# Performance work log

Hardware: AMD Instinct MI355X
Metric: run time of the kernel (lower is better)

The kernel has to match this reference:

```python
import jax, jax.numpy as jnp
import numpy as np

LN_EPS = 1e-5


def setup_inputs() -> dict:
    key = jax.random.key(0)
    ks = jax.random.split(key, 5)
    L, G, D, E = 2, 50000, 128, 800000
    x = jax.random.normal(ks[0], (L, G, D), dtype=jnp.float32)
    rows = jax.random.randint(ks[1], (E,), 0, G, dtype=jnp.int32)
    cols = jax.random.randint(ks[2], (E,), 0, G, dtype=jnp.int32)
    vals = jax.random.uniform(ks[3], (E,), dtype=jnp.float32)
    W = jax.random.normal(ks[4], (D, D), dtype=jnp.float32) * 0.05
    b = jnp.zeros((D,), dtype=jnp.float32)
    gamma = jnp.ones((D,), dtype=jnp.float32)
    beta = jnp.zeros((D,), dtype=jnp.float32)
    return {"x": x, "rows": rows, "cols": cols, "vals": vals,
            "W": W, "b": b, "gamma": gamma, "beta": beta}


def reference(x, rows, cols, vals, W, b, gamma, beta):
    L, G, D = x.shape
    # sparse connection_matrix @ x, edge-list form (COO): out[r] += v * x_t[c]
    xt = x.transpose(1, 0, 2).reshape(G, L * D)          # [G, L*D]
    msg = xt[cols] * vals[:, None]                        # [E, L*D]
    agg = jax.ops.segment_sum(msg, rows, num_segments=G)  # [G, L*D]
    y = agg.reshape(G, L, D).transpose(1, 0, 2)           # [L, G, D]
    # linear + SiLU
    h = jnp.einsum('lgd,od->lgo', y, W) + b
    s = h * jax.nn.sigmoid(h)
    # LayerNorm over last dim
    mu = jnp.mean(s, axis=-1, keepdims=True)
    var = jnp.mean(jnp.square(s - mu), axis=-1, keepdims=True)
    out = (s - mu) * jax.lax.rsqrt(var + LN_EPS) * gamma + beta
    return out
```

## Files before the change

### kernel.cpp

```cpp
#include <hip/hip_runtime.h>
#include <hip/hip_bf16.h>
#include <math.h>

typedef short bf16x8 __attribute__((ext_vector_type(8)));
typedef float f32x4 __attribute__((ext_vector_type(4)));

#define SPW 2
#define CAP 64
#define CSTR 16

static __device__ __forceinline__ float bf2f(ushort u) {
  union { unsigned i; float f; } c;
  c.i = ((unsigned)u) << 16;
  return c.f;
}

static __device__ __forceinline__ ushort f2bf(float f) {
  __hip_bfloat16 h = __float2bfloat16(f);
  return *reinterpret_cast<ushort*>(&h);
}

__global__ __launch_bounds__(256) void prep_kernel(const float* __restrict__ W,
                                                   ushort* __restrict__ Wb,
                                                   int* __restrict__ counts,
                                                   int n_counts) {
  int t = blockIdx.x * 256 + threadIdx.x;
  if (t < 16384) Wb[t] = f2bf(W[t]);
  for (int i = t; i < n_counts; i += (int)gridDim.x * 256) counts[i] = 0;
}

__global__ __launch_bounds__(256) void bucket_kernel(
    const int* __restrict__ rows, const int* __restrict__ cols,
    const float* __restrict__ vals, int* __restrict__ counts,
    int2* __restrict__ ev, int E) {
  int e = blockIdx.x * 256 + threadIdx.x;
  if (e >= E) return;
  int r = rows[e];
  int pos = atomicAdd(&counts[r * CSTR], 1);
  if (pos < CAP)
    ev[(size_t)r * CAP + pos] = make_int2(cols[e] << 8, __float_as_int(vals[e]));
}

__global__ __launch_bounds__(256) void zgemm_kernel(
    const float* __restrict__ x, const ushort* __restrict__ Wb,
    ushort* __restrict__ zb, int nstripes) {
  const int lane = threadIdx.x & 63;
  const int wid = blockIdx.x * 4 + (threadIdx.x >> 6);

  const int o_lo = lane & 15;
  const int kg = lane >> 4;

  bf16x8 wf[8][4];
#pragma unroll
  for (int on = 0; on < 8; ++on)
#pragma unroll
    for (int kc = 0; kc < 4; ++kc)
      wf[on][kc] = *reinterpret_cast<const bf16x8*>(
          Wb + (size_t)(on * 16 + o_lo) * 128 + kc * 32 + kg * 8);

  for (int i = 0; i < SPW; ++i) {
    const int s = wid * SPW + i;
    if (s >= nstripes) return;
    const int row0 = s << 4;

    bf16x8 af[4];
#pragma unroll
    for (int kc = 0; kc < 4; ++kc) {
      const float* src = x + (size_t)(row0 + o_lo) * 128 + kc * 32 + kg * 8;
      float4 v0 = *reinterpret_cast<const float4*>(src);
      float4 v1 = *reinterpret_cast<const float4*>(src + 4);
      bf16x8 t;
      t[0] = (short)f2bf(v0.x); t[1] = (short)f2bf(v0.y);
      t[2] = (short)f2bf(v0.z); t[3] = (short)f2bf(v0.w);
      t[4] = (short)f2bf(v1.x); t[5] = (short)f2bf(v1.y);
      t[6] = (short)f2bf(v1.z); t[7] = (short)f2bf(v1.w);
      af[kc] = t;
    }

    f32x4 acc[8];
#pragma unroll
    for (int on = 0; on < 8; ++on) acc[on] = (f32x4){0.f, 0.f, 0.f, 0.f};

#pragma unroll
    for (int kc = 0; kc < 4; ++kc)
#pragma unroll
      for (int on = 0; on < 8; ++on)
        acc[on] = __builtin_amdgcn_mfma_f32_16x16x32_bf16(wf[on][kc], af[kc],
                                                          acc[on], 0, 0, 0);

    ushort* zr = zb + (size_t)(row0 + o_lo) * 128 + kg * 4;
#pragma unroll
    for (int on = 0; on < 8; ++on) {
      ushort4 st;
      st.x = f2bf(acc[on][0]);
      st.y = f2bf(acc[on][1]);
      st.z = f2bf(acc[on][2]);
      st.w = f2bf(acc[on][3]);
      *reinterpret_cast<ushort4*>(zr + on * 16) = st;
    }
  }
}

__global__ __launch_bounds__(256) void gather_fused_kernel(
    const ushort* __restrict__ zb, const int* __restrict__ counts,
    const int2* __restrict__ ev, const float* __restrict__ b,
    const float* __restrict__ gamma, const float* __restrict__ beta,
    float* __restrict__ out, int G, int GD) {
  int g = blockIdx.x * 4 + (threadIdx.x >> 6);
  if (g >= G) return;
  const int lane = threadIdx.x & 63;
  const int l = lane >> 5;
  const int q = lane & 31;
  const char* zbase = (const char*)(zb + (size_t)l * GD);
  const uint qoff = (uint)q << 3;

  const int2* evr = ev + (size_t)g * CAP;
  int n = counts[g * CSTR];
  if (n > CAP) n = CAP;
  float4 acc = make_float4(0.f, 0.f, 0.f, 0.f);

  int i = 0;
  for (; i + 3 < n; i += 4) {
    int2 e0 = evr[i], e1 = evr[i + 1], e2 = evr[i + 2], e3 = evr[i + 3];
    ushort4 a0 = *reinterpret_cast<const ushort4*>(zbase + ((uint)e0.x + qoff));
    ushort4 a1 = *reinterpret_cast<const ushort4*>(zbase + ((uint)e1.x + qoff));
    ushort4 a2 = *reinterpret_cast<const ushort4*>(zbase + ((uint)e2.x + qoff));
    ushort4 a3 = *reinterpret_cast<const ushort4*>(zbase + ((uint)e3.x + qoff));
    float v0 = __int_as_float(e0.y), v1 = __int_as_float(e1.y);
    float v2 = __int_as_float(e2.y), v3 = __int_as_float(e3.y);
    acc.x += v0 * bf2f(a0.x) + v1 * bf2f(a1.x) + v2 * bf2f(a2.x) + v3 * bf2f(a3.x);
    acc.y += v0 * bf2f(a0.y) + v1 * bf2f(a1.y) + v2 * bf2f(a2.y) + v3 * bf2f(a3.y);
    acc.z += v0 * bf2f(a0.z) + v1 * bf2f(a1.z) + v2 * bf2f(a2.z) + v3 * bf2f(a3.z);
    acc.w += v0 * bf2f(a0.w) + v1 * bf2f(a1.w) + v2 * bf2f(a2.w) + v3 * bf2f(a3.w);
  }
  for (; i < n; ++i) {
    int2 e0 = evr[i];
    float v0 = __int_as_float(e0.y);
    ushort4 a0 = *reinterpret_cast<const ushort4*>(zbase + ((uint)e0.x + qoff));
    acc.x += v0 * bf2f(a0.x);
    acc.y += v0 * bf2f(a0.y);
    acc.z += v0 * bf2f(a0.z);
    acc.w += v0 * bf2f(a0.w);
  }

  const int d0 = q * 4;
  const float4 bb = *reinterpret_cast<const float4*>(b + d0);
  float4 s;
  {
    float h0 = acc.x + bb.x, h1 = acc.y + bb.y;
    float h2 = acc.z + bb.z, h3 = acc.w + bb.w;
    s.x = h0 / (1.f + expf(-h0));
    s.y = h1 / (1.f + expf(-h1));
    s.z = h2 / (1.f + expf(-h2));
    s.w = h3 / (1.f + expf(-h3));
  }
  float sum = s.x + s.y + s.z + s.w;
  float sq = s.x * s.x + s.y * s.y + s.z * s.z + s.w * s.w;
#pragma unroll
  for (int m = 1; m <= 16; m <<= 1) {
    sum += __shfl_xor(sum, m);
    sq += __shfl_xor(sq, m);
  }
  const float mu = sum * (1.f / 128.f);
  const float var = sq * (1.f / 128.f) - mu * mu;
  const float inv = rsqrtf(var + 1e-5f);
  const float4 gm = *reinterpret_cast<const float4*>(gamma + d0);
  const float4 bt = *reinterpret_cast<const float4*>(beta + d0);
  float4 o;
  o.x = (s.x - mu) * inv * gm.x + bt.x;
  o.y = (s.y - mu) * inv * gm.y + bt.y;
  o.z = (s.z - mu) * inv * gm.z + bt.z;
  o.w = (s.w - mu) * inv * gm.w + bt.w;
  *reinterpret_cast<float4*>(out + (size_t)l * GD + (size_t)g * 128 + d0) = o;
}

extern "C" void kernel_launch(void* const* d_in, const int* in_sizes, int n_in,
                              void* d_out, int out_size, void* d_ws,
                              size_t ws_size, hipStream_t stream) {
  const float* x = (const float*)d_in[0];
  const int* rows = (const int*)d_in[1];
  const int* cols = (const int*)d_in[2];
  const float* vals = (const float*)d_in[3];
  const float* W = (const float*)d_in[4];
  const float* b = (const float*)d_in[5];
  const float* gamma = (const float*)d_in[6];
  const float* beta = (const float*)d_in[7];

  const int E = in_sizes[1];
  const int G = in_sizes[0] / 256;
  const int GD = G * 128;

  char* ws = (char*)d_ws;
  ushort* zb = (ushort*)ws;
  int* counts = (int*)(zb + (size_t)2 * GD);
  ushort* Wb = (ushort*)(counts + (size_t)G * CSTR);
  int2* ev = (int2*)(Wb + 16384);

  prep_kernel<<<256, 256, 0, stream>>>(W, Wb, counts, G * CSTR);
  bucket_kernel<<<(E + 255) / 256, 256, 0, stream>>>(rows, cols, vals, counts,
                                                     ev, E);
  const int nstripes = (G * 2) / 16;
  zgemm_kernel<<<(nstripes + 4 * SPW - 1) / (4 * SPW), 256, 0, stream>>>(
      x, Wb, zb, nstripes);
  gather_fused_kernel<<<(G + 3) / 4, 256, 0, stream>>>(zb, counts, ev, b,
                                                       gamma, beta,
                                                       (float*)d_out, G, GD);
}
```

Before: 146.6 us.

## Replicate edge buckets per block group and pack edges into 32-bit words

Edges are scattered into 8 replicated bucket sets, chosen by block index, so that atomics on the same row's counter contend less. Each edge is packed into one 32-bit word holding a bf16 value and a 17-bit column index, which halves edge-list traffic. The cost is a counts array that needs more zeroing, eight count loads and short serial loops per row in the gather, and lost ILP from dropping the 4-way unroll. It also lowers edge values to bf16 precision and caps each replica at 16 edges.

After: 194.2 us. 32.5% more time.

```diff
diff --git a/kernel.cpp b/kernel.cpp
--- a/kernel.cpp
+++ b/kernel.cpp
@@ -6,8 +6,9 @@
 typedef float f32x4 __attribute__((ext_vector_type(4)));
 
 #define SPW 2
-#define CAP 64
-#define CSTR 16
+#define NREP 8
+#define CAPR 16
+#define CSTR 4
 
 static __device__ __forceinline__ float bf2f(ushort u) {
   union { unsigned i; float f; } c;
@@ -32,13 +33,17 @@
 __global__ __launch_bounds__(256) void bucket_kernel(
     const int* __restrict__ rows, const int* __restrict__ cols,
     const float* __restrict__ vals, int* __restrict__ counts,
-    int2* __restrict__ ev, int E) {
+    uint* __restrict__ ev, int E, int G) {
   int e = blockIdx.x * 256 + threadIdx.x;
   if (e >= E) return;
+  const int rep = blockIdx.x & (NREP - 1);
   int r = rows[e];
-  int pos = atomicAdd(&counts[r * CSTR], 1);
-  if (pos < CAP)
-    ev[(size_t)r * CAP + pos] = make_int2(cols[e] << 8, __float_as_int(vals[e]));
+  const size_t rr = (size_t)rep * G + r;
+  int pos = atomicAdd(&counts[rr * CSTR], 1);
+  if (pos < CAPR) {
+    uint u = ((uint)f2bf(vals[e]) << 17) | (uint)cols[e];
+    ev[rr * CAPR + pos] = u;
+  }
 }
 
 __global__ __launch_bounds__(256) void zgemm_kernel(
@@ -103,7 +108,7 @@
 
 __global__ __launch_bounds__(256) void gather_fused_kernel(
     const ushort* __restrict__ zb, const int* __restrict__ counts,
-    const int2* __restrict__ ev, const float* __restrict__ b,
+    const uint* __restrict__ ev, const float* __restrict__ b,
     const float* __restrict__ gamma, const float* __restrict__ beta,
     float* __restrict__ out, int G, int GD) {
   int g = blockIdx.x * 4 + (threadIdx.x >> 6);
@@ -114,33 +119,26 @@
   const char* zbase = (const char*)(zb + (size_t)l * GD);
   const uint qoff = (uint)q << 3;
 
-  const int2* evr = ev + (size_t)g * CAP;
-  int n = counts[g * CSTR];
-  if (n > CAP) n = CAP;
   float4 acc = make_float4(0.f, 0.f, 0.f, 0.f);
 
-  int i = 0;
-  for (; i + 3 < n; i += 4) {
-    int2 e0 = evr[i], e1 = evr[i + 1], e2 = evr[i + 2], e3 = evr[i + 3];
-    ushort4 a0 = *reinterpret_cast<const ushort4*>(zbase + ((uint)e0.x + qoff));
-    ushort4 a1 = *reinterpret_cast<const ushort4*>(zbase + ((uint)e1.x + qoff));
-    ushort4 a2 = *reinterpret_cast<const ushort4*>(zbase + ((uint)e2.x + qoff));
-    ushort4 a3 = *reinterpret_cast<const ushort4*>(zbase + ((uint)e3.x + qoff));
-    float v0 = __int_as_float(e0.y), v1 = __int_as_float(e1.y);
-    float v2 = __int_as_float(e2.y), v3 = __int_as_float(e3.y);
-    acc.x += v0 * bf2f(a0.x) + v1 * bf2f(a1.x) + v2 * bf2f(a2.x) + v3 * bf2f(a3.x);
-    acc.y += v0 * bf2f(a0.y) + v1 * bf2f(a1.y) + v2 * bf2f(a2.y) + v3 * bf2f(a3.y);
-    acc.z += v0 * bf2f(a0.z) + v1 * bf2f(a1.z) + v2 * bf2f(a2.z) + v3 * bf2f(a3.z);
-    acc.w += v0 * bf2f(a0.w) + v1 * bf2f(a1.w) + v2 * bf2f(a2.w) + v3 * bf2f(a3.w);
-  }
-  for (; i < n; ++i) {
-    int2 e0 = evr[i];
-    float v0 = __int_as_float(e0.y);
-    ushort4 a0 = *reinterpret_cast<const ushort4*>(zbase + ((uint)e0.x + qoff));
-    acc.x += v0 * bf2f(a0.x);
-    acc.y += v0 * bf2f(a0.y);
-    acc.z += v0 * bf2f(a0.z);
-    acc.w += v0 * bf2f(a0.w);
+#pragma unroll
+  for (int rep = 0; rep < NREP; ++rep) {
+    const size_t rr = (size_t)rep * G + g;
+    int n = counts[rr * CSTR];
+    if (n > CAPR) n = CAPR;
+    const uint* evr = ev + rr * CAPR;
+    for (int j = 0; j < n; ++j) {
+      const uint u = evr[j];
+      union { uint i; float f; } cv;
+      cv.i = (u >> 17) << 16;
+      const float v = cv.f;
+      const ushort4 a = *reinterpret_cast<const ushort4*>(
+          zbase + ((u & 0x1FFFFu) << 8) + qoff);
+      acc.x += v * bf2f(a.x);
+      acc.y += v * bf2f(a.y);
+      acc.z += v * bf2f(a.z);
+      acc.w += v * bf2f(a.w);
+    }
   }
 
   const int d0 = q * 4;
@@ -193,12 +191,12 @@
   char* ws = (char*)d_ws;
   ushort* zb = (ushort*)ws;
   int* counts = (int*)(zb + (size_t)2 * GD);
-  ushort* Wb = (ushort*)(counts + (size_t)G * CSTR);
-  int2* ev = (int2*)(Wb + 16384);
-
-  prep_kernel<<<256, 256, 0, stream>>>(W, Wb, counts, G * CSTR);
+  ushort* Wb = (ushort*)(counts + (size_t)NREP * G * CSTR);
+  uint* ev = (uint*)(Wb + 16384);
+
+  prep_kernel<<<1024, 256, 0, stream>>>(W, Wb, counts, NREP * G * CSTR);
   bucket_kernel<<<(E + 255) / 256, 256, 0, stream>>>(rows, cols, vals, counts,
-                                                     ev, E);
+                                                     ev, E, G);
   const int nstripes = (G * 2) / 16;
   zgemm_kernel<<<(nstripes + 4 * SPW - 1) / (4 * SPW), 256, 0, stream>>>(
       x, Wb, zb, nstripes);
```
